# Optimization experiments

Measured on AMD Instinct MI355X. Metric: run time of the kernel, lower is better.

The kernel has to match this reference:

```python
import jax, jax.numpy as jnp
import numpy as np

N = 100000      # num nodes
E = 1600000     # num edges
DIN, DH, DOUT = 128, 64, 32
BN_EPS = 1e-5


def setup_inputs() -> dict:
    key = jax.random.key(0)
    ks = jax.random.split(key, 6)

    def xavier(k, fi, fo):
        lim = np.sqrt(6.0 / (fi + fo)).astype(np.float32)
        return jax.random.uniform(k, (fi, fo), jnp.float32, -lim, lim)

    return {
        "x": jax.random.normal(ks[0], (N, DIN), jnp.float32),
        "edge_index": jax.random.randint(ks[1], (2, E), 0, N, dtype=jnp.int32),
        "W1": xavier(ks[2], DIN, DH),
        "b1": jnp.zeros((DH,), jnp.float32),
        "gamma1": jnp.ones((DH,), jnp.float32),
        "beta1": jnp.zeros((DH,), jnp.float32),
        "W2": xavier(ks[3], DH, DOUT),
        "b2": jnp.zeros((DOUT,), jnp.float32),
    }


def _gcn_norm(edge_index, n, dtype):
    # add self-loops, then symmetric normalization deg^-1/2[src] * deg^-1/2[dst]
    loop = jnp.arange(n, dtype=edge_index.dtype)
    src = jnp.concatenate([edge_index[0], loop])
    dst = jnp.concatenate([edge_index[1], loop])
    deg = jax.ops.segment_sum(jnp.ones_like(dst, dtype=dtype), dst, num_segments=n)
    dis = 1.0 / jnp.sqrt(deg)  # deg >= 1 due to self-loops
    norm = dis[src] * dis[dst]
    return src, dst, norm


def _gcn_layer(h, W, b, src, dst, norm, n):
    h = h @ W
    msg = h[src] * norm[:, None]                       # [E+N, d] gather
    out = jax.ops.segment_sum(msg, dst, num_segments=n)  # scatter-add
    return out + b


def reference(x, edge_index, W1, b1, gamma1, beta1, W2, b2):
    src, dst, norm = _gcn_norm(edge_index, N, x.dtype)
    # layer 1: GCNConv -> BatchNorm (batch stats) -> ReLU (dropout = eval/identity)
    h = _gcn_layer(x, W1, b1, src, dst, norm, N)
    mean = h.mean(axis=0)
    var = h.var(axis=0)
    h = (h - mean) / jnp.sqrt(var + BN_EPS) * gamma1 + beta1
    h = jax.nn.relu(h)
    # layer 2: GCNConv -> node embeddings [N, DOUT]
    out = _gcn_layer(h, W2, b2, src, dst, norm, N)
    return out
```

## Files before the change

kernel.cpp:

```cpp
#include <hip/hip_runtime.h>

#define DIN 128
#define DH 64
#define DOUT 32
#define BN_EPS 1e-5f

#define BK 128
#define BKSH 7
#define NBK_MAX 784
#define G 256
#define CAP 2560

typedef __attribute__((ext_vector_type(8))) short short8;
typedef __attribute__((ext_vector_type(4))) float floatx4;

__device__ __forceinline__ unsigned short f2bf(float f) {
    union { float f; unsigned u; } v; v.f = f;
    unsigned r = (v.u + 0x7FFFu + ((v.u >> 16) & 1u)) >> 16;
    return (unsigned short)r;
}
__device__ __forceinline__ float bf2f(unsigned short h) {
    union { unsigned u; float f; } v; v.u = ((unsigned)h) << 16;
    return v.f;
}
__device__ __forceinline__ float lo_f(unsigned u) {
    union { unsigned u; float f; } v; v.u = u << 16;
    return v.f;
}
__device__ __forceinline__ float hi_f(unsigned u) {
    union { unsigned u; float f; } v; v.u = u & 0xFFFF0000u;
    return v.f;
}
__device__ __forceinline__ unsigned pack2bf(float lo, float hi) {
    return (unsigned)f2bf(lo) | ((unsigned)f2bf(hi) << 16);
}


__global__ __launch_bounds__(512) void hist_k(const int* __restrict__ dst, int* __restrict__ hist_g,
                                              int E, int nbk, int chunk) {
    __shared__ int hist[NBK_MAX];
    int g = blockIdx.x, tid = threadIdx.x;
    for (int b = tid; b < nbk; b += 512) hist[b] = 0;
    __syncthreads();
    int i0 = g * chunk, iend = min(i0 + chunk, E);
    for (int i = i0 + tid; i < iend; i += 512)
        atomicAdd(&hist[dst[i] >> BKSH], 1);
    __syncthreads();
    for (int b = tid; b < nbk; b += 512)
        hist_g[(size_t)g * nbk + b] = hist[b];
}


__global__ __launch_bounds__(256) void scan_k(const int* __restrict__ hist_g, int* __restrict__ rowoff,
                                              int* __restrict__ tot, int nbk) {
    __shared__ int seg[16][17];
    int tid = threadIdx.x;
    int gl = tid >> 4, bl = tid & 15;
    int b = blockIdx.x * 16 + bl;
    bool bok = b < nbk;
    int vals[16];
    int psum = 0;
    #pragma unroll
    for (int j = 0; j < 16; j++) {
        int g = gl * 16 + j;
        int v = bok ? hist_g[(size_t)g * nbk + b] : 0;
        vals[j] = v; psum += v;
    }
    seg[gl][bl] = psum;
    __syncthreads();
    #pragma unroll
    for (int off = 1; off < 16; off <<= 1) {
        int t = (gl >= off) ? seg[gl - off][bl] : 0;
        __syncthreads();
        seg[gl][bl] += t;
        __syncthreads();
    }
    int run = seg[gl][bl] - psum;
    if (gl == 15 && bok) tot[b] = seg[15][bl];
    #pragma unroll
    for (int j = 0; j < 16; j++) {
        int g = gl * 16 + j;
        if (bok) rowoff[(size_t)g * nbk + b] = run;
        run += vals[j];
    }
}


__global__ __launch_bounds__(512) void scatter_k(const int* __restrict__ src, const int* __restrict__ dst,
                                                 const int* __restrict__ rowoff,
                                                 unsigned* __restrict__ recs, int E, int nbk, int chunk) {
    __shared__ int cur[NBK_MAX];
    int g = blockIdx.x, tid = threadIdx.x;
    for (int b = tid; b < nbk; b += 512)
        cur[b] = b * CAP + rowoff[(size_t)g * nbk + b];
    __syncthreads();
    int i0 = g * chunk, iend = min(i0 + chunk, E);
    for (int i = i0 + tid; i < iend; i += 512) {
        int s = src[i], d = dst[i];
        int b = d >> BKSH;
        int slot = atomicAdd(&cur[b], 1);
        if (slot < (b + 1) * CAP)
            recs[slot] = ((unsigned)s << BKSH) | (unsigned)(d & (BK - 1));
    }
}


__global__ __launch_bounds__(512) void csr_k(const unsigned* __restrict__ recs, const int* __restrict__ tot,
                                             float* __restrict__ dis, int2* __restrict__ rpde,
                                             int* __restrict__ col, int n) {
    __shared__ int deg8[8][BK];
    __shared__ int wb[8][BK];
    __shared__ int deg[BK], sc[BK], bas[BK];
    int b = blockIdx.x, tid = threadIdx.x;
    int w = tid >> 6, lane = tid & 63;
    for (int i = tid; i < 8 * BK; i += 512) ((int*)deg8)[i] = 0;
    __syncthreads();
    int lo = b * CAP;
    int ne = min(tot[b], CAP);
    int hi = lo + ne;
    for (int e = lo + w * 64 + lane; e < hi; e += 512)
        atomicAdd(&deg8[w][recs[e] & (BK - 1)], 1);
    __syncthreads();
    if (tid < BK) {
        int run = 0;
        #pragma unroll
        for (int ww = 0; ww < 8; ww++) { wb[ww][tid] = run; run += deg8[ww][tid]; }
        deg[tid] = run; sc[tid] = run;
    }
    __syncthreads();
    for (int off = 1; off < BK; off <<= 1) {
        int t = (tid < BK && tid >= off) ? sc[tid - off] : 0;
        __syncthreads();
        if (tid < BK) sc[tid] += t;
        __syncthreads();
    }
    if (tid < BK) {
        bas[tid] = sc[tid] - deg[tid];
        int g = b * BK + tid;
        if (g < n) {
            dis[g] = rsqrtf((float)(deg[tid] + 1));
            rpde[g] = make_int2(lo + bas[tid], deg[tid]);
        }
    }
    __syncthreads();
    for (int i = tid; i < 8 * BK; i += 512)
        ((int*)wb)[i] += bas[i & (BK - 1)];
    __syncthreads();
    for (int e = lo + w * 64 + lane; e < hi; e += 512) {
        unsigned r = recs[e];
        int dl = r & (BK - 1);
        int k = atomicAdd(&wb[w][dl], 1);
        col[lo + k] = (int)(r >> BKSH);
    }
}


__global__ __launch_bounds__(256) void gemm1_k(const float* __restrict__ x,
                                               const float* __restrict__ W1,
                                               const float* __restrict__ dis,
                                               unsigned short* __restrict__ h1s, int n) {
    __shared__ unsigned short xb[64][136];
    __shared__ unsigned short wt[64][136];
    int tid = threadIdx.x;
    int r0b = blockIdx.x * 64;

    for (int c = tid; c < 2048; c += 256) {
        int k = c >> 4, n4 = (c & 15) * 4;
        float4 v = ((const float4*)W1)[c];
        wt[n4 + 0][k] = f2bf(v.x);
        wt[n4 + 1][k] = f2bf(v.y);
        wt[n4 + 2][k] = f2bf(v.z);
        wt[n4 + 3][k] = f2bf(v.w);
    }
    for (int c = tid; c < 2048; c += 256) {
        int r = c >> 5, k4 = (c & 31) * 4;
        int gr = r0b + r;
        float4 v = make_float4(0.f, 0.f, 0.f, 0.f);
        if (gr < n) v = ((const float4*)x)[(gr << 5) + (k4 >> 2)];
        ushort4 o;
        o.x = f2bf(v.x); o.y = f2bf(v.y); o.z = f2bf(v.z); o.w = f2bf(v.w);
        *(ushort4*)&xb[r][k4] = o;
    }
    __syncthreads();

    int w = tid >> 6, lane = tid & 63;
    int rr = lane & 15, q = lane >> 4;
    floatx4 acc0 = {0.f, 0.f, 0.f, 0.f}, acc1 = acc0, acc2 = acc0, acc3 = acc0;
    #pragma unroll
    for (int kt = 0; kt < 4; kt++) {
        int k0 = kt * 32 + q * 8;
        short8 a  = *(const short8*)&xb[w * 16 + rr][k0];
        short8 b0 = *(const short8*)&wt[rr][k0];
        short8 b1 = *(const short8*)&wt[16 + rr][k0];
        short8 b2 = *(const short8*)&wt[32 + rr][k0];
        short8 b3 = *(const short8*)&wt[48 + rr][k0];
        acc0 = __builtin_amdgcn_mfma_f32_16x16x32_bf16(a, b0, acc0, 0, 0, 0);
        acc1 = __builtin_amdgcn_mfma_f32_16x16x32_bf16(a, b1, acc1, 0, 0, 0);
        acc2 = __builtin_amdgcn_mfma_f32_16x16x32_bf16(a, b2, acc2, 0, 0, 0);
        acc3 = __builtin_amdgcn_mfma_f32_16x16x32_bf16(a, b3, acc3, 0, 0, 0);
    }
    #pragma unroll
    for (int t = 0; t < 4; t++) {
        int gr = r0b + w * 16 + q * 4 + t;
        if (gr < n) {
            float dd = dis[gr];
            unsigned short* o = &h1s[gr * 64];
            o[rr]      = f2bf(acc0[t] * dd);
            o[16 + rr] = f2bf(acc1[t] * dd);
            o[32 + rr] = f2bf(acc2[t] * dd);
            o[48 + rr] = f2bf(acc3[t] * dd);
        }
    }
}


__global__ __launch_bounds__(256) void agg1_k(const unsigned* __restrict__ h1p,
                                              const int2* __restrict__ rpde,
                                              const int* __restrict__ col,
                                              unsigned* __restrict__ outp, int n) {
    int node = (blockIdx.x * 256 + threadIdx.x) >> 6;
    int lane = threadIdx.x & 63;
    if (node >= n) return;
    int f2 = lane & 31, eslot = lane >> 5;
    int2 rd = rpde[node];
    int e  = __builtin_amdgcn_readfirstlane(rd.x);
    int dg = __builtin_amdgcn_readfirstlane(rd.y);

    float lo0 = 0.f, lo1 = 0.f, lo2 = 0.f, lo3 = 0.f, lo4 = 0.f, lo5 = 0.f, lo6 = 0.f, lo7 = 0.f;
    float hi0 = 0.f, hi1 = 0.f, hi2 = 0.f, hi3 = 0.f, hi4 = 0.f, hi5 = 0.f, hi6 = 0.f, hi7 = 0.f;
    int b = 0;
    for (; b + 16 <= dg; b += 16) {
        int s0 = col[e + b + 0 + eslot],  s1 = col[e + b + 2 + eslot];
        int s2 = col[e + b + 4 + eslot],  s3 = col[e + b + 6 + eslot];
        int s4 = col[e + b + 8 + eslot],  s5 = col[e + b + 10 + eslot];
        int s6 = col[e + b + 12 + eslot], s7 = col[e + b + 14 + eslot];
        unsigned u0 = h1p[s0 * 32 + f2], u1 = h1p[s1 * 32 + f2];
        unsigned u2 = h1p[s2 * 32 + f2], u3 = h1p[s3 * 32 + f2];
        unsigned u4 = h1p[s4 * 32 + f2], u5 = h1p[s5 * 32 + f2];
        unsigned u6 = h1p[s6 * 32 + f2], u7 = h1p[s7 * 32 + f2];
        lo0 += lo_f(u0); hi0 += hi_f(u0);
        lo1 += lo_f(u1); hi1 += hi_f(u1);
        lo2 += lo_f(u2); hi2 += hi_f(u2);
        lo3 += lo_f(u3); hi3 += hi_f(u3);
        lo4 += lo_f(u4); hi4 += hi_f(u4);
        lo5 += lo_f(u5); hi5 += hi_f(u5);
        lo6 += lo_f(u6); hi6 += hi_f(u6);
        lo7 += lo_f(u7); hi7 += hi_f(u7);
    }
    if (b < dg) {
        int last = dg - 1;
        int i0 = b + 0 + eslot,  i1 = b + 2 + eslot,  i2 = b + 4 + eslot,  i3 = b + 6 + eslot;
        int i4 = b + 8 + eslot,  i5 = b + 10 + eslot, i6 = b + 12 + eslot, i7 = b + 14 + eslot;
        int s0 = col[e + min(i0, last)], s1 = col[e + min(i1, last)];
        int s2 = col[e + min(i2, last)], s3 = col[e + min(i3, last)];
        int s4 = col[e + min(i4, last)], s5 = col[e + min(i5, last)];
        int s6 = col[e + min(i6, last)], s7 = col[e + min(i7, last)];
        unsigned u0 = h1p[s0 * 32 + f2], u1 = h1p[s1 * 32 + f2];
        unsigned u2 = h1p[s2 * 32 + f2], u3 = h1p[s3 * 32 + f2];
        unsigned u4 = h1p[s4 * 32 + f2], u5 = h1p[s5 * 32 + f2];
        unsigned u6 = h1p[s6 * 32 + f2], u7 = h1p[s7 * 32 + f2];
        lo0 += (i0 < dg) ? lo_f(u0) : 0.f; hi0 += (i0 < dg) ? hi_f(u0) : 0.f;
        lo1 += (i1 < dg) ? lo_f(u1) : 0.f; hi1 += (i1 < dg) ? hi_f(u1) : 0.f;
        lo2 += (i2 < dg) ? lo_f(u2) : 0.f; hi2 += (i2 < dg) ? hi_f(u2) : 0.f;
        lo3 += (i3 < dg) ? lo_f(u3) : 0.f; hi3 += (i3 < dg) ? hi_f(u3) : 0.f;
        lo4 += (i4 < dg) ? lo_f(u4) : 0.f; hi4 += (i4 < dg) ? hi_f(u4) : 0.f;
        lo5 += (i5 < dg) ? lo_f(u5) : 0.f; hi5 += (i5 < dg) ? hi_f(u5) : 0.f;
        lo6 += (i6 < dg) ? lo_f(u6) : 0.f; hi6 += (i6 < dg) ? hi_f(u6) : 0.f;
        lo7 += (i7 < dg) ? lo_f(u7) : 0.f; hi7 += (i7 < dg) ? hi_f(u7) : 0.f;
    }
    float lo = ((lo0 + lo1) + (lo2 + lo3)) + ((lo4 + lo5) + (lo6 + lo7));
    float hi = ((hi0 + hi1) + (hi2 + hi3)) + ((hi4 + hi5) + (hi6 + hi7));
    lo += __shfl_xor(lo, 32, 64);
    hi += __shfl_xor(hi, 32, 64);
    if (eslot == 0) {
        unsigned us = h1p[node * 32 + f2];
        float dn = rsqrtf((float)(dg + 1));
        outp[node * 32 + f2] = pack2bf((lo + lo_f(us)) * dn, (hi + hi_f(us)) * dn);
    }
}


__global__ __launch_bounds__(256) void bnstats_k(const unsigned short* __restrict__ agg1b,
                                                 float* __restrict__ stats, int n) {
    int f = threadIdx.x & 63, g = threadIdx.x >> 6;
    float sum = 0.f, sq = 0.f;
    for (int r = blockIdx.x * 4 + g; r < n; r += gridDim.x * 4) {
        float v = bf2f(agg1b[r * 64 + f]);
        sum += v; sq += v * v;
    }
    __shared__ float s1[4][64], s2[4][64];
    s1[g][f] = sum; s2[g][f] = sq;
    __syncthreads();
    if (g == 0) {
        sum = s1[0][f] + s1[1][f] + s1[2][f] + s1[3][f];
        sq  = s2[0][f] + s2[1][f] + s2[2][f] + s2[3][f];
        atomicAdd(&stats[f], sum);
        atomicAdd(&stats[64 + f], sq);
    }
}


__global__ __launch_bounds__(256) void gemm2_k(const unsigned short* __restrict__ agg1b,
                                               const float* __restrict__ W2,
                                               const float* __restrict__ stats,
                                               const float* __restrict__ gamma, const float* __restrict__ beta,
                                               const float* __restrict__ dis,
                                               unsigned short* __restrict__ h2s, float invn, int n) {
    __shared__ unsigned short ab[64][72];
    __shared__ unsigned short wt[32][72];
    __shared__ float s_s[64], s_t[64];
    int tid = threadIdx.x;
    int r0b = blockIdx.x * 64;
    if (tid < 64) {
        float mean = stats[tid] * invn;
        float var = stats[64 + tid] * invn - mean * mean;
        float s = gamma[tid] * rsqrtf(var + BN_EPS);
        s_s[tid] = s;
        s_t[tid] = beta[tid] - mean * s;
    }
    for (int c = tid; c < 512; c += 256) {
        int k = c >> 3, n4 = (c & 7) * 4;
        float4 v = ((const float4*)W2)[c];
        wt[n4 + 0][k] = f2bf(v.x);
        wt[n4 + 1][k] = f2bf(v.y);
        wt[n4 + 2][k] = f2bf(v.z);
        wt[n4 + 3][k] = f2bf(v.w);
    }
    __syncthreads();
    for (int c = tid; c < 512; c += 256) {
        int r = c >> 3, k0 = (c & 7) * 8;
        int gr = r0b + r;
        unsigned short tmp[8];
        if (gr < n) {
            const unsigned short* ap = &agg1b[gr * 64 + k0];
            #pragma unroll
            for (int j = 0; j < 8; j++)
                tmp[j] = f2bf(fmaxf(bf2f(ap[j]) * s_s[k0 + j] + s_t[k0 + j], 0.f));
        } else {
            #pragma unroll
            for (int j = 0; j < 8; j++) tmp[j] = 0;
        }
        *(short8*)&ab[r][k0] = *(short8*)tmp;
    }
    __syncthreads();

    int w = tid >> 6, lane = tid & 63;
    int rr = lane & 15, q = lane >> 4;
    floatx4 acc0 = {0.f, 0.f, 0.f, 0.f}, acc1 = acc0;
    #pragma unroll
    for (int kt = 0; kt < 2; kt++) {
        int k0 = kt * 32 + q * 8;
        short8 a  = *(const short8*)&ab[w * 16 + rr][k0];
        short8 b0 = *(const short8*)&wt[rr][k0];
        short8 b1 = *(const short8*)&wt[16 + rr][k0];
        acc0 = __builtin_amdgcn_mfma_f32_16x16x32_bf16(a, b0, acc0, 0, 0, 0);
        acc1 = __builtin_amdgcn_mfma_f32_16x16x32_bf16(a, b1, acc1, 0, 0, 0);
    }
    #pragma unroll
    for (int t = 0; t < 4; t++) {
        int gr = r0b + w * 16 + q * 4 + t;
        if (gr < n) {
            float dd = dis[gr];
            h2s[gr * 32 + rr]      = f2bf(acc0[t] * dd);
            h2s[gr * 32 + 16 + rr] = f2bf(acc1[t] * dd);
        }
    }
}


__global__ __launch_bounds__(256) void agg2_k(const unsigned* __restrict__ h2p,
                                              const int2* __restrict__ rpde,
                                              const int* __restrict__ col, const float* __restrict__ b2,
                                              float* __restrict__ out, int n) {
    int wave = (blockIdx.x * 256 + threadIdx.x) >> 6;
    int lane = threadIdx.x & 63;
    int half = lane >> 5, hl = lane & 31;
    int node = wave * 2 + half;
    if (node >= n) return;
    int f2 = hl & 15, eslot = hl >> 4;
    int2 rd = rpde[node];
    int e = rd.x, dg = rd.y;

    float lo0 = 0.f, lo1 = 0.f, lo2 = 0.f, lo3 = 0.f, lo4 = 0.f, lo5 = 0.f, lo6 = 0.f, lo7 = 0.f;
    float hi0 = 0.f, hi1 = 0.f, hi2 = 0.f, hi3 = 0.f, hi4 = 0.f, hi5 = 0.f, hi6 = 0.f, hi7 = 0.f;
    int b = 0;
    for (; b + 16 <= dg; b += 16) {
        int s0 = col[e + b + 0 + eslot],  s1 = col[e + b + 2 + eslot];
        int s2 = col[e + b + 4 + eslot],  s3 = col[e + b + 6 + eslot];
        int s4 = col[e + b + 8 + eslot],  s5 = col[e + b + 10 + eslot];
        int s6 = col[e + b + 12 + eslot], s7 = col[e + b + 14 + eslot];
        unsigned u0 = h2p[s0 * 16 + f2], u1 = h2p[s1 * 16 + f2];
        unsigned u2 = h2p[s2 * 16 + f2], u3 = h2p[s3 * 16 + f2];
        unsigned u4 = h2p[s4 * 16 + f2], u5 = h2p[s5 * 16 + f2];
        unsigned u6 = h2p[s6 * 16 + f2], u7 = h2p[s7 * 16 + f2];
        lo0 += lo_f(u0); hi0 += hi_f(u0);
        lo1 += lo_f(u1); hi1 += hi_f(u1);
        lo2 += lo_f(u2); hi2 += hi_f(u2);
        lo3 += lo_f(u3); hi3 += hi_f(u3);
        lo4 += lo_f(u4); hi4 += hi_f(u4);
        lo5 += lo_f(u5); hi5 += hi_f(u5);
        lo6 += lo_f(u6); hi6 += hi_f(u6);
        lo7 += lo_f(u7); hi7 += hi_f(u7);
    }
    if (b < dg) {
        int last = dg - 1;
        int i0 = b + 0 + eslot,  i1 = b + 2 + eslot,  i2 = b + 4 + eslot,  i3 = b + 6 + eslot;
        int i4 = b + 8 + eslot,  i5 = b + 10 + eslot, i6 = b + 12 + eslot, i7 = b + 14 + eslot;
        int s0 = col[e + min(i0, last)], s1 = col[e + min(i1, last)];
        int s2 = col[e + min(i2, last)], s3 = col[e + min(i3, last)];
        int s4 = col[e + min(i4, last)], s5 = col[e + min(i5, last)];
        int s6 = col[e + min(i6, last)], s7 = col[e + min(i7, last)];
        unsigned u0 = h2p[s0 * 16 + f2], u1 = h2p[s1 * 16 + f2];
        unsigned u2 = h2p[s2 * 16 + f2], u3 = h2p[s3 * 16 + f2];
        unsigned u4 = h2p[s4 * 16 + f2], u5 = h2p[s5 * 16 + f2];
        unsigned u6 = h2p[s6 * 16 + f2], u7 = h2p[s7 * 16 + f2];
        lo0 += (i0 < dg) ? lo_f(u0) : 0.f; hi0 += (i0 < dg) ? hi_f(u0) : 0.f;
        lo1 += (i1 < dg) ? lo_f(u1) : 0.f; hi1 += (i1 < dg) ? hi_f(u1) : 0.f;
        lo2 += (i2 < dg) ? lo_f(u2) : 0.f; hi2 += (i2 < dg) ? hi_f(u2) : 0.f;
        lo3 += (i3 < dg) ? lo_f(u3) : 0.f; hi3 += (i3 < dg) ? hi_f(u3) : 0.f;
        lo4 += (i4 < dg) ? lo_f(u4) : 0.f; hi4 += (i4 < dg) ? hi_f(u4) : 0.f;
        lo5 += (i5 < dg) ? lo_f(u5) : 0.f; hi5 += (i5 < dg) ? hi_f(u5) : 0.f;
        lo6 += (i6 < dg) ? lo_f(u6) : 0.f; hi6 += (i6 < dg) ? hi_f(u6) : 0.f;
        lo7 += (i7 < dg) ? lo_f(u7) : 0.f; hi7 += (i7 < dg) ? hi_f(u7) : 0.f;
    }
    float lo = ((lo0 + lo1) + (lo2 + lo3)) + ((lo4 + lo5) + (lo6 + lo7));
    float hi = ((hi0 + hi1) + (hi2 + hi3)) + ((hi4 + hi5) + (hi6 + hi7));
    lo += __shfl_xor(lo, 16, 64);
    hi += __shfl_xor(hi, 16, 64);
    if (eslot == 0) {
        unsigned us = h2p[node * 16 + f2];
        float dn = rsqrtf((float)(dg + 1));
        float2 bb = ((const float2*)b2)[f2];
        float2 o;
        o.x = (lo + lo_f(us)) * dn + bb.x;
        o.y = (hi + hi_f(us)) * dn + bb.y;
        ((float2*)out)[node * 16 + f2] = o;
    }
}


extern "C" void kernel_launch(void* const* d_in, const int* in_sizes, int n_in,
                              void* d_out, int out_size, void* d_ws, size_t ws_size,
                              hipStream_t stream) {
    const float* x      = (const float*)d_in[0];
    const int*   ei     = (const int*)d_in[1];
    const float* W1     = (const float*)d_in[2];
    const float* gamma1 = (const float*)d_in[4];
    const float* beta1  = (const float*)d_in[5];
    const float* W2     = (const float*)d_in[6];
    const float* b2     = (const float*)d_in[7];
    float* out = (float*)d_out;

    int N = in_sizes[0] / DIN;
    int E = in_sizes[1] / 2;
    const int* src = ei;
    const int* dst = ei + E;
    int nbk = (N + BK - 1) >> BKSH;
    int chunk = (E + G - 1) / G;

    size_t off = 0;
    auto alloc = [&](size_t elems) -> void* {
        void* p = (char*)d_ws + off * 4;
        off += (elems + 127) & ~size_t(127);
        return p;
    };
    int*            hist_g = (int*)alloc((size_t)G * NBK_MAX);
    int*            rowoff = (int*)alloc((size_t)G * NBK_MAX);
    int*            tot    = (int*)alloc(NBK_MAX);
    unsigned*       recs   = (unsigned*)alloc((size_t)NBK_MAX * CAP);
    int*            col    = (int*)alloc((size_t)NBK_MAX * CAP);
    float*          dis    = (float*)alloc(N);
    int2*           rpde   = (int2*)alloc((size_t)N * 2);
    float*          stats  = (float*)alloc(128);
    unsigned short* h1s    = (unsigned short*)alloc((size_t)N * DH / 2);
    unsigned short* agg1b  = (unsigned short*)alloc((size_t)N * DH / 2);
    unsigned short* h2s    = h1s;

    hipMemsetAsync(stats, 0, 128 * sizeof(float), stream);

    hist_k<<<G, 512, 0, stream>>>(dst, hist_g, E, nbk, chunk);
    scan_k<<<(nbk + 15) / 16, 256, 0, stream>>>(hist_g, rowoff, tot, nbk);
    scatter_k<<<G, 512, 0, stream>>>(src, dst, rowoff, recs, E, nbk, chunk);
    csr_k<<<nbk, 512, 0, stream>>>(recs, tot, dis, rpde, col, N);

    gemm1_k<<<(N + 63) / 64, 256, 0, stream>>>(x, W1, dis, h1s, N);
    agg1_k<<<(N + 3) / 4, 256, 0, stream>>>((const unsigned*)h1s, rpde, col, (unsigned*)agg1b, N);

    bnstats_k<<<400, 256, 0, stream>>>(agg1b, stats, N);

    gemm2_k<<<(N + 63) / 64, 256, 0, stream>>>(agg1b, W2, stats, gamma1, beta1, dis, h2s,
                                               1.0f / (float)N, N);
    agg2_k<<<(N + 7) / 8, 256, 0, stream>>>((const unsigned*)h2s, rpde, col, b2, out, N);
}
```

Measured before the change: 251.8 us.

## Pad CSR rows to multiples of 8 with zero dummy node; vectorize aggregation gathers

```diff
diff --git a/kernel.cpp b/kernel.cpp
--- a/kernel.cpp
+++ b/kernel.cpp
@@ -10,6 +10,7 @@
 #define NBK_MAX 784
 #define G 256
 #define CAP 2560
+#define CCAP 3584
 
 typedef __attribute__((ext_vector_type(8))) short short8;
 typedef __attribute__((ext_vector_type(4))) float floatx4;
@@ -116,6 +117,7 @@
     for (int i = tid; i < 8 * BK; i += 512) ((int*)deg8)[i] = 0;
     __syncthreads();
     int lo = b * CAP;
+    int clo = b * CCAP;
     int ne = min(tot[b], CAP);
     int hi = lo + ne;
     for (int e = lo + w * 64 + lane; e < hi; e += 512)
@@ -125,7 +127,8 @@
         int run = 0;
         #pragma unroll
         for (int ww = 0; ww < 8; ww++) { wb[ww][tid] = run; run += deg8[ww][tid]; }
-        deg[tid] = run; sc[tid] = run;
+        deg[tid] = run;
+        sc[tid] = (run + 7) & ~7;
     }
     __syncthreads();
     for (int off = 1; off < BK; off <<= 1) {
@@ -135,12 +138,17 @@
         __syncthreads();
     }
     if (tid < BK) {
-        bas[tid] = sc[tid] - deg[tid];
+        int d = deg[tid];
+        int pdeg = (d + 7) & ~7;
+        int base = sc[tid] - pdeg;
+        bas[tid] = base;
         int g = b * BK + tid;
         if (g < n) {
-            dis[g] = rsqrtf((float)(deg[tid] + 1));
-            rpde[g] = make_int2(lo + bas[tid], deg[tid]);
+            dis[g] = rsqrtf((float)(d + 1));
+            rpde[g] = make_int2(clo + base, d);
         }
+        for (int j = d; j < pdeg; j++)
+            col[clo + base + j] = n;
     }
     __syncthreads();
     for (int i = tid; i < 8 * BK; i += 512)
@@ -150,7 +158,7 @@
         unsigned r = recs[e];
         int dl = r & (BK - 1);
         int k = atomicAdd(&wb[w][dl], 1);
-        col[lo + k] = (int)(r >> BKSH);
+        col[clo + k] = (int)(r >> BKSH);
     }
 }
 
@@ -209,6 +217,9 @@
             o[16 + rr] = f2bf(acc1[t] * dd);
             o[32 + rr] = f2bf(acc2[t] * dd);
             o[48 + rr] = f2bf(acc3[t] * dd);
+        } else if (gr == n) {
+            unsigned short* o = &h1s[gr * 64];
+            o[rr] = 0; o[16 + rr] = 0; o[32 + rr] = 0; o[48 + rr] = 0;
         }
     }
 }
@@ -221,61 +232,41 @@
     int node = (blockIdx.x * 256 + threadIdx.x) >> 6;
     int lane = threadIdx.x & 63;
     if (node >= n) return;
-    int f2 = lane & 31, eslot = lane >> 5;
+    int f2 = lane & 15, eslot = lane >> 4;
     int2 rd = rpde[node];
     int e  = __builtin_amdgcn_readfirstlane(rd.x);
     int dg = __builtin_amdgcn_readfirstlane(rd.y);
-
-    float lo0 = 0.f, lo1 = 0.f, lo2 = 0.f, lo3 = 0.f, lo4 = 0.f, lo5 = 0.f, lo6 = 0.f, lo7 = 0.f;
-    float hi0 = 0.f, hi1 = 0.f, hi2 = 0.f, hi3 = 0.f, hi4 = 0.f, hi5 = 0.f, hi6 = 0.f, hi7 = 0.f;
-    int b = 0;
-    for (; b + 16 <= dg; b += 16) {
-        int s0 = col[e + b + 0 + eslot],  s1 = col[e + b + 2 + eslot];
-        int s2 = col[e + b + 4 + eslot],  s3 = col[e + b + 6 + eslot];
-        int s4 = col[e + b + 8 + eslot],  s5 = col[e + b + 10 + eslot];
-        int s6 = col[e + b + 12 + eslot], s7 = col[e + b + 14 + eslot];
-        unsigned u0 = h1p[s0 * 32 + f2], u1 = h1p[s1 * 32 + f2];
-        unsigned u2 = h1p[s2 * 32 + f2], u3 = h1p[s3 * 32 + f2];
-        unsigned u4 = h1p[s4 * 32 + f2], u5 = h1p[s5 * 32 + f2];
-        unsigned u6 = h1p[s6 * 32 + f2], u7 = h1p[s7 * 32 + f2];
-        lo0 += lo_f(u0); hi0 += hi_f(u0);
-        lo1 += lo_f(u1); hi1 += hi_f(u1);
-        lo2 += lo_f(u2); hi2 += hi_f(u2);
-        lo3 += lo_f(u3); hi3 += hi_f(u3);
-        lo4 += lo_f(u4); hi4 += hi_f(u4);
-        lo5 += lo_f(u5); hi5 += hi_f(u5);
-        lo6 += lo_f(u6); hi6 += hi_f(u6);
-        lo7 += lo_f(u7); hi7 += hi_f(u7);
-    }
-    if (b < dg) {
-        int last = dg - 1;
-        int i0 = b + 0 + eslot,  i1 = b + 2 + eslot,  i2 = b + 4 + eslot,  i3 = b + 6 + eslot;
-        int i4 = b + 8 + eslot,  i5 = b + 10 + eslot, i6 = b + 12 + eslot, i7 = b + 14 + eslot;
-        int s0 = col[e + min(i0, last)], s1 = col[e + min(i1, last)];
-        int s2 = col[e + min(i2, last)], s3 = col[e + min(i3, last)];
-        int s4 = col[e + min(i4, last)], s5 = col[e + min(i5, last)];
-        int s6 = col[e + min(i6, last)], s7 = col[e + min(i7, last)];
-        unsigned u0 = h1p[s0 * 32 + f2], u1 = h1p[s1 * 32 + f2];
-        unsigned u2 = h1p[s2 * 32 + f2], u3 = h1p[s3 * 32 + f2];
-        unsigned u4 = h1p[s4 * 32 + f2], u5 = h1p[s5 * 32 + f2];
-        unsigned u6 = h1p[s6 * 32 + f2], u7 = h1p[s7 * 32 + f2];
-        lo0 += (i0 < dg) ? lo_f(u0) : 0.f; hi0 += (i0 < dg) ? hi_f(u0) : 0.f;
-        lo1 += (i1 < dg) ? lo_f(u1) : 0.f; hi1 += (i1 < dg) ? hi_f(u1) : 0.f;
-        lo2 += (i2 < dg) ? lo_f(u2) : 0.f; hi2 += (i2 < dg) ? hi_f(u2) : 0.f;
-        lo3 += (i3 < dg) ? lo_f(u3) : 0.f; hi3 += (i3 < dg) ? hi_f(u3) : 0.f;
-        lo4 += (i4 < dg) ? lo_f(u4) : 0.f; hi4 += (i4 < dg) ? hi_f(u4) : 0.f;
-        lo5 += (i5 < dg) ? lo_f(u5) : 0.f; hi5 += (i5 < dg) ? hi_f(u5) : 0.f;
-        lo6 += (i6 < dg) ? lo_f(u6) : 0.f; hi6 += (i6 < dg) ? hi_f(u6) : 0.f;
-        lo7 += (i7 < dg) ? lo_f(u7) : 0.f; hi7 += (i7 < dg) ? hi_f(u7) : 0.f;
-    }
-    float lo = ((lo0 + lo1) + (lo2 + lo3)) + ((lo4 + lo5) + (lo6 + lo7));
-    float hi = ((hi0 + hi1) + (hi2 + hi3)) + ((hi4 + hi5) + (hi6 + hi7));
-    lo += __shfl_xor(lo, 32, 64);
-    hi += __shfl_xor(hi, 32, 64);
+    int pdg = (dg + 7) & ~7;
+
+    const uint2* h1q = (const uint2*)h1p;
+    float l0x = 0.f, h0x = 0.f, l0y = 0.f, h0y = 0.f;
+    float l1x = 0.f, h1x = 0.f, l1y = 0.f, h1y = 0.f;
+    int c0 = n, c1 = n;
+    if (pdg > 0) { c0 = col[e + eslot]; c1 = col[e + 4 + eslot]; }
+    for (int b = 0; b < pdg; b += 8) {
+        uint2 u0 = h1q[c0 * 16 + f2];
+        uint2 u1 = h1q[c1 * 16 + f2];
+        int bn = (b + 8 < pdg) ? b + 8 : b;
+        c0 = col[e + bn + eslot];
+        c1 = col[e + bn + 4 + eslot];
+        l0x += lo_f(u0.x); h0x += hi_f(u0.x);
+        l0y += lo_f(u0.y); h0y += hi_f(u0.y);
+        l1x += lo_f(u1.x); h1x += hi_f(u1.x);
+        l1y += lo_f(u1.y); h1y += hi_f(u1.y);
+    }
+    float ax = l0x + l1x, bx = h0x + h1x;
+    float ay = l0y + l1y, by = h0y + h1y;
+    ax += __shfl_xor(ax, 16, 64); ax += __shfl_xor(ax, 32, 64);
+    bx += __shfl_xor(bx, 16, 64); bx += __shfl_xor(bx, 32, 64);
+    ay += __shfl_xor(ay, 16, 64); ay += __shfl_xor(ay, 32, 64);
+    by += __shfl_xor(by, 16, 64); by += __shfl_xor(by, 32, 64);
     if (eslot == 0) {
-        unsigned us = h1p[node * 32 + f2];
+        uint2 us = h1q[node * 16 + f2];
         float dn = rsqrtf((float)(dg + 1));
-        outp[node * 32 + f2] = pack2bf((lo + lo_f(us)) * dn, (hi + hi_f(us)) * dn);
+        uint2 o;
+        o.x = pack2bf((ax + lo_f(us.x)) * dn, (bx + hi_f(us.x)) * dn);
+        o.y = pack2bf((ay + lo_f(us.y)) * dn, (by + hi_f(us.y)) * dn);
+        ((uint2*)outp)[node * 16 + f2] = o;
     }
 }
 
@@ -363,6 +354,9 @@
             float dd = dis[gr];
             h2s[gr * 32 + rr]      = f2bf(acc0[t] * dd);
             h2s[gr * 32 + 16 + rr] = f2bf(acc1[t] * dd);
+        } else if (gr == n) {
+            h2s[gr * 32 + rr]      = 0;
+            h2s[gr * 32 + 16 + rr] = 0;
         }
     }
 }
@@ -377,64 +371,43 @@
     int half = lane >> 5, hl = lane & 31;
     int node = wave * 2 + half;
     if (node >= n) return;
-    int f2 = hl & 15, eslot = hl >> 4;
+    int f2 = hl & 7, eslot = hl >> 3;
     int2 rd = rpde[node];
     int e = rd.x, dg = rd.y;
-
-    float lo0 = 0.f, lo1 = 0.f, lo2 = 0.f, lo3 = 0.f, lo4 = 0.f, lo5 = 0.f, lo6 = 0.f, lo7 = 0.f;
-    float hi0 = 0.f, hi1 = 0.f, hi2 = 0.f, hi3 = 0.f, hi4 = 0.f, hi5 = 0.f, hi6 = 0.f, hi7 = 0.f;
-    int b = 0;
-    for (; b + 16 <= dg; b += 16) {
-        int s0 = col[e + b + 0 + eslot],  s1 = col[e + b + 2 + eslot];
-        int s2 = col[e + b + 4 + eslot],  s3 = col[e + b + 6 + eslot];
-        int s4 = col[e + b + 8 + eslot],  s5 = col[e + b + 10 + eslot];
-        int s6 = col[e + b + 12 + eslot], s7 = col[e + b + 14 + eslot];
-        unsigned u0 = h2p[s0 * 16 + f2], u1 = h2p[s1 * 16 + f2];
-        unsigned u2 = h2p[s2 * 16 + f2], u3 = h2p[s3 * 16 + f2];
-        unsigned u4 = h2p[s4 * 16 + f2], u5 = h2p[s5 * 16 + f2];
-        unsigned u6 = h2p[s6 * 16 + f2], u7 = h2p[s7 * 16 + f2];
-        lo0 += lo_f(u0); hi0 += hi_f(u0);
-        lo1 += lo_f(u1); hi1 += hi_f(u1);
-        lo2 += lo_f(u2); hi2 += hi_f(u2);
-        lo3 += lo_f(u3); hi3 += hi_f(u3);
-        lo4 += lo_f(u4); hi4 += hi_f(u4);
-        lo5 += lo_f(u5); hi5 += hi_f(u5);
-        lo6 += lo_f(u6); hi6 += hi_f(u6);
-        lo7 += lo_f(u7); hi7 += hi_f(u7);
-    }
-    if (b < dg) {
-        int last = dg - 1;
-        int i0 = b + 0 + eslot,  i1 = b + 2 + eslot,  i2 = b + 4 + eslot,  i3 = b + 6 + eslot;
-        int i4 = b + 8 + eslot,  i5 = b + 10 + eslot, i6 = b + 12 + eslot, i7 = b + 14 + eslot;
-        int s0 = col[e + min(i0, last)], s1 = col[e + min(i1, last)];
-        int s2 = col[e + min(i2, last)], s3 = col[e + min(i3, last)];
-        int s4 = col[e + min(i4, last)], s5 = col[e + min(i5, last)];
-        int s6 = col[e + min(i6, last)], s7 = col[e + min(i7, last)];
-        unsigned u0 = h2p[s0 * 16 + f2], u1 = h2p[s1 * 16 + f2];
-        unsigned u2 = h2p[s2 * 16 + f2], u3 = h2p[s3 * 16 + f2];
-        unsigned u4 = h2p[s4 * 16 + f2], u5 = h2p[s5 * 16 + f2];
-        unsigned u6 = h2p[s6 * 16 + f2], u7 = h2p[s7 * 16 + f2];
-        lo0 += (i0 < dg) ? lo_f(u0) : 0.f; hi0 += (i0 < dg) ? hi_f(u0) : 0.f;
-        lo1 += (i1 < dg) ? lo_f(u1) : 0.f; hi1 += (i1 < dg) ? hi_f(u1) : 0.f;
-        lo2 += (i2 < dg) ? lo_f(u2) : 0.f; hi2 += (i2 < dg) ? hi_f(u2) : 0.f;
-        lo3 += (i3 < dg) ? lo_f(u3) : 0.f; hi3 += (i3 < dg) ? hi_f(u3) : 0.f;
-        lo4 += (i4 < dg) ? lo_f(u4) : 0.f; hi4 += (i4 < dg) ? hi_f(u4) : 0.f;
-        lo5 += (i5 < dg) ? lo_f(u5) : 0.f; hi5 += (i5 < dg) ? hi_f(u5) : 0.f;
-        lo6 += (i6 < dg) ? lo_f(u6) : 0.f; hi6 += (i6 < dg) ? hi_f(u6) : 0.f;
-        lo7 += (i7 < dg) ? lo_f(u7) : 0.f; hi7 += (i7 < dg) ? hi_f(u7) : 0.f;
-    }
-    float lo = ((lo0 + lo1) + (lo2 + lo3)) + ((lo4 + lo5) + (lo6 + lo7));
-    float hi = ((hi0 + hi1) + (hi2 + hi3)) + ((hi4 + hi5) + (hi6 + hi7));
-    lo += __shfl_xor(lo, 16, 64);
-    hi += __shfl_xor(hi, 16, 64);
+    int pdg = (dg + 7) & ~7;
+
+    const uint2* h2q = (const uint2*)h2p;
+    float l0x = 0.f, h0x = 0.f, l0y = 0.f, h0y = 0.f;
+    float l1x = 0.f, h1x = 0.f, l1y = 0.f, h1y = 0.f;
+    int c0 = n, c1 = n;
+    if (pdg > 0) { c0 = col[e + eslot]; c1 = col[e + 4 + eslot]; }
+    for (int b = 0; b < pdg; b += 8) {
+        uint2 u0 = h2q[c0 * 8 + f2];
+        uint2 u1 = h2q[c1 * 8 + f2];
+        int bn = (b + 8 < pdg) ? b + 8 : b;
+        c0 = col[e + bn + eslot];
+        c1 = col[e + bn + 4 + eslot];
+        l0x += lo_f(u0.x); h0x += hi_f(u0.x);
+        l0y += lo_f(u0.y); h0y += hi_f(u0.y);
+        l1x += lo_f(u1.x); h1x += hi_f(u1.x);
+        l1y += lo_f(u1.y); h1y += hi_f(u1.y);
+    }
+    float ax = l0x + l1x, bx = h0x + h1x;
+    float ay = l0y + l1y, by = h0y + h1y;
+    ax += __shfl_xor(ax, 8, 64); ax += __shfl_xor(ax, 16, 64);
+    bx += __shfl_xor(bx, 8, 64); bx += __shfl_xor(bx, 16, 64);
+    ay += __shfl_xor(ay, 8, 64); ay += __shfl_xor(ay, 16, 64);
+    by += __shfl_xor(by, 8, 64); by += __shfl_xor(by, 16, 64);
     if (eslot == 0) {
-        unsigned us = h2p[node * 16 + f2];
+        uint2 us = h2q[node * 8 + f2];
         float dn = rsqrtf((float)(dg + 1));
-        float2 bb = ((const float2*)b2)[f2];
-        float2 o;
-        o.x = (lo + lo_f(us)) * dn + bb.x;
-        o.y = (hi + hi_f(us)) * dn + bb.y;
-        ((float2*)out)[node * 16 + f2] = o;
+        float4 bb = ((const float4*)b2)[f2];
+        float4 o;
+        o.x = (ax + lo_f(us.x)) * dn + bb.x;
+        o.y = (bx + hi_f(us.x)) * dn + bb.y;
+        o.z = (ay + lo_f(us.y)) * dn + bb.z;
+        o.w = (by + hi_f(us.y)) * dn + bb.w;
+        ((float4*)out)[node * 8 + f2] = o;
     }
 }
 
@@ -468,11 +441,11 @@
     int*            rowoff = (int*)alloc((size_t)G * NBK_MAX);
     int*            tot    = (int*)alloc(NBK_MAX);
     unsigned*       recs   = (unsigned*)alloc((size_t)NBK_MAX * CAP);
-    int*            col    = (int*)alloc((size_t)NBK_MAX * CAP);
+    int*            col    = (int*)alloc((size_t)NBK_MAX * CCAP);
     float*          dis    = (float*)alloc(N);
     int2*           rpde   = (int2*)alloc((size_t)N * 2);
     float*          stats  = (float*)alloc(128);
-    unsigned short* h1s    = (unsigned short*)alloc((size_t)N * DH / 2);
+    unsigned short* h1s    = (unsigned short*)alloc((size_t)(N + 1) * DH / 2);
     unsigned short* agg1b  = (unsigned short*)alloc((size_t)N * DH / 2);
     unsigned short* h2s    = h1s;
 
```

New measurement: 259.0 us. 1.03x slower.
